# Kernel tuning notes

Measured on AMD Instinct MI355X. Metric: run time of the kernel, lower is better.

Reference implementation:

```python
import jax, jax.numpy as jnp
import numpy as np

B, L, H, K = 16, 65536, 64, 64


def setup_inputs() -> dict:
    key = jax.random.key(0)
    k1, k2 = jax.random.split(key, 2)
    x = jax.random.normal(k1, (B, L), dtype=jnp.float32)
    W = jax.random.normal(k2, (K, H), dtype=jnp.float32) * 0.02  # nn.Linear weight [K, H]
    b = jnp.zeros((K,), dtype=jnp.float32)
    return {"x": x, "W": W, "b": b}


def reference(x, W, b):
    # x: [B, L]; W: [K, H]; b: [K]
    Hh = W.shape[1]
    Bb, Ll = x.shape
    xpad = jnp.pad(x, ((0, 0), (Hh - 1, 0)))  # left-pad like F.pad(x, (H-1, 0))
    # Hankel windows: windows[b, t, j] = xpad[b, t + j]  -> [B, L, H]
    idx = jnp.arange(Ll)[:, None] + jnp.arange(Hh)[None, :]
    windows = xpad[:, idx]
    mu = windows.mean(axis=2, keepdims=True)
    sd = windows.std(axis=2, keepdims=True, ddof=1)  # torch std is unbiased (ddof=1)
    wn = (windows - mu) / (sd + 1e-6)
    d2 = jax.nn.relu(jnp.einsum('blh,kh->blk', wn, W) + b)
    warmup = Hh - 1
    return (d2[:, warmup:, :], warmup)
```

## Files before the change

kernel.cpp:

```cpp
#include <hip/hip_runtime.h>
#include <hip/hip_bf16.h>
#include <stdint.h>

#define LCOUNT 65536
#define LOUT   65473
#define KF     64
#define HH     64
#define TL     1024
#define ROW4   1104

typedef __attribute__((ext_vector_type(8))) short  short8;
typedef __attribute__((ext_vector_type(4))) short  short4v;
typedef __attribute__((ext_vector_type(4))) float  float4v;
typedef __attribute__((ext_vector_type(2))) float  float2v;

__device__ __forceinline__ unsigned short f2bf(float f) {
    union { float f; uint32_t u; } c; c.f = f;
    uint32_t u = c.u;
    u += 0x7FFFu + ((u >> 16) & 1u);
    return (unsigned short)(u >> 16);
}

__global__ __launch_bounds__(256, 4)
void hankel_kernel(const float* __restrict__ x,
                   const float* __restrict__ W,
                   const float* __restrict__ bias,
                   float* __restrict__ out)
{
    __shared__ __align__(16) float          xs_f[TL + 64];
    __shared__ __align__(16) unsigned short rep4[4 * ROW4];
    __shared__ __align__(16) float          muinv_s[2 * TL];
    __shared__ float wsum_s[KF];
    __shared__ float bias_s[KF];

    const int tid  = threadIdx.x;
    const int lane = tid & 63;
    const int wv   = tid >> 6;
    const int m    = lane & 15;
    const int quad = lane >> 4;

    const int tile     = blockIdx.x;
    const int bb       = blockIdx.y;
    const int block_lo = tile * TL;

    {
        const float4v* xrow4 = (const float4v*)(x + (size_t)bb * LCOUNT);
        const int base4 = block_lo >> 2;
        const int nf4   = (TL + 64) / 4;
        for (int i4 = tid; i4 < nf4; i4 += 256) {
            int g4 = base4 + i4;
            if (g4 > LCOUNT / 4 - 1) g4 = LCOUNT / 4 - 1;
            float4v v = xrow4[g4];
            *(float4v*)(xs_f + 4 * i4) = v;
            uint32_t plo = (uint32_t)f2bf(v[0]) | ((uint32_t)f2bf(v[1]) << 16);
            uint32_t phi = (uint32_t)f2bf(v[2]) | ((uint32_t)f2bf(v[3]) << 16);
            *(uint2*)(rep4 + 4 * i4) = make_uint2(plo, phi);
        }
    }

    if (tid < KF) {
        const float4v* wr = (const float4v*)(W + tid * HH);
        float s = 0.f;
        #pragma unroll
        for (int i = 0; i < HH / 4; ++i) {
            float4v w = wr[i];
            s += w[0] + w[1] + w[2] + w[3];
        }
        wsum_s[tid] = s;
        bias_s[tid] = bias[tid];
    }

    short8 afrag[4][2];
    #pragma unroll
    for (int t = 0; t < 4; ++t) {
        const int k = t * 16 + m;
        #pragma unroll
        for (int ki = 0; ki < 2; ++ki) {
            const float4v* wp = (const float4v*)(W + k * HH + quad * 8 + ki * 32);
            float4v w0 = wp[0];
            float4v w1 = wp[1];
            short8 f;
            f[0] = (short)f2bf(w0[0]); f[1] = (short)f2bf(w0[1]);
            f[2] = (short)f2bf(w0[2]); f[3] = (short)f2bf(w0[3]);
            f[4] = (short)f2bf(w1[0]); f[5] = (short)f2bf(w1[1]);
            f[6] = (short)f2bf(w1[2]); f[7] = (short)f2bf(w1[3]);
            afrag[t][ki] = f;
        }
    }

    __syncthreads();

    {
        const int p0 = 4 * tid;
        const float4v* xv = (const float4v*)(xs_f + p0);
        float s1 = 0.f, s2 = 0.f;
        float4v v0 = xv[0];
        float4v v16 = xv[16];
        #pragma unroll
        for (int i = 0; i < 16; ++i) {
            float4v v = xv[i];
            s1 += v[0] + v[1] + v[2] + v[3];
            s2 += v[0] * v[0] + v[1] * v[1] + v[2] * v[2] + v[3] * v[3];
        }
        float mu4[4], inv4[4];
        #pragma unroll
        for (int i = 0; i < 4; ++i) {
            if (i > 0) {
                float xo = v0[i - 1], xn = v16[i - 1];
                s1 += xn - xo;
                s2 += xn * xn - xo * xo;
            }
            float mu  = s1 * (1.f / 64.f);
            float var = (s2 - 64.f * mu * mu) * (1.f / 63.f);
            var = var < 0.f ? 0.f : var;
            mu4[i]  = mu;
            inv4[i] = 1.f / (sqrtf(var) + 1e-6f);
        }
        float4v lo4, hi4;
        lo4[0] = mu4[0]; lo4[1] = inv4[0]; lo4[2] = mu4[1]; lo4[3] = inv4[1];
        hi4[0] = mu4[2]; hi4[1] = inv4[2]; hi4[2] = mu4[3]; hi4[3] = inv4[3];
        *(float4v*)(muinv_s + 8 * tid)     = lo4;
        *(float4v*)(muinv_s + 8 * tid + 4) = hi4;
    }

    for (int tt = tid; tt < 544; tt += 256) {
        const int s = tt & 3;
        const int c = tt >> 2;
        if (s) {
            const int i0 = 8 * c + s;
            short8 w;
            #pragma unroll
            for (int j = 0; j < 8; ++j) w[j] = (short)rep4[i0 + j];
            *(short8*)(rep4 + s * ROW4 + 8 * c) = w;
        }
    }
    __syncthreads();

    const unsigned short* myrow = rep4 + (m & 3) * ROW4 + (m & 12) + quad * 8;
    float* const outb = out + (size_t)bb * LOUT * KF + quad * 4;

    for (int gg = wv; gg < TL / 16; gg += 8) {
        float4v pay[2][4];
        #pragma unroll
        for (int u = 0; u < 2; ++u) {
            const int g  = gg + 4 * u;
            const int p0 = g * 16;

            short4v a0 = *(const short4v*)(myrow + p0);
            short4v a1 = *(const short4v*)(myrow + p0 + 4);
            short4v a2 = *(const short4v*)(myrow + p0 + 32);
            short4v a3 = *(const short4v*)(myrow + p0 + 36);
            short8 b0 = __builtin_shufflevector(a0, a1, 0, 1, 2, 3, 4, 5, 6, 7);
            short8 b1 = __builtin_shufflevector(a2, a3, 0, 1, 2, 3, 4, 5, 6, 7);

            float2v mi = *(const float2v*)(muinv_s + 2 * (p0 + m));
            const float invv = mi[1];
            const float nmi  = -mi[0] * invv;

            float4v acc[4];
            #pragma unroll
            for (int t = 0; t < 4; ++t) acc[t] = (float4v){0.f, 0.f, 0.f, 0.f};
            #pragma unroll
            for (int t = 0; t < 4; ++t) {
                acc[t] = __builtin_amdgcn_mfma_f32_16x16x32_bf16(afrag[t][0], b0, acc[t], 0, 0, 0);
                acc[t] = __builtin_amdgcn_mfma_f32_16x16x32_bf16(afrag[t][1], b1, acc[t], 0, 0, 0);
            }

            #pragma unroll
            for (int t = 0; t < 4; ++t) {
                float4v ws = *(const float4v*)(wsum_s + t * 16 + quad * 4);
                float4v bs = *(const float4v*)(bias_s + t * 16 + quad * 4);
                #pragma unroll
                for (int r = 0; r < 4; ++r) {
                    float vv = fmaf(acc[t][r], invv, fmaf(nmi, ws[r], bs[r]));
                    pay[u][t][r] = vv > 0.f ? vv : 0.f;
                }
            }

            const int pos = block_lo + p0 + m;
            if (pos < LOUT) {
                float* op = outb + (size_t)pos * KF;
                #pragma unroll
                for (int t = 0; t < 4; ++t)
                    __builtin_nontemporal_store(pay[u][t], (float4v*)(op + t * 16));
            }
        }
    }

    if (tile == 0 && bb == 0 && tid == 0) {
        out[(size_t)16 * LOUT * KF] = 63.0f;
    }
}

extern "C" void kernel_launch(void* const* d_in, const int* in_sizes, int n_in,
                              void* d_out, int out_size, void* d_ws, size_t ws_size,
                              hipStream_t stream) {
    const float* x = (const float*)d_in[0];
    const float* W = (const float*)d_in[1];
    const float* b = (const float*)d_in[2];
    float* out = (float*)d_out;

    dim3 grid((LOUT + TL - 1) / TL, 16);
    hankel_kernel<<<grid, 256, 0, stream>>>(x, W, b, out);
}
```

Before: 311.7 us.

## Halve tile size, raise occupancy, and use plain stores instead of nontemporal

Shrinks the per-block tile from 1024 to 512 positions and raises the launch-bounds occupancy hint from 4 to 8 blocks per CU. The shared-memory setup loops become single guarded passes. The main loop drops the two-group software unroll and processes one 16-position group per iteration, storing each result right after compute with regular stores instead of nontemporal stores. The aim is more concurrent blocks to hide latency on this store-bound kernel, at the cost of more halo reloads, more per-block setup, and losing the nontemporal cache hint.

New measurement: 368.9 us. +18.3%, slower.

```diff
diff --git a/kernel.cpp b/kernel.cpp
--- a/kernel.cpp
+++ b/kernel.cpp
@@ -6,8 +6,8 @@
 #define LOUT   65473
 #define KF     64
 #define HH     64
-#define TL     1024
-#define ROW4   1104
+#define TL     512
+#define ROW4   592
 
 typedef __attribute__((ext_vector_type(8))) short  short8;
 typedef __attribute__((ext_vector_type(4))) short  short4v;
@@ -21,7 +21,7 @@
     return (unsigned short)(u >> 16);
 }
 
-__global__ __launch_bounds__(256, 4)
+__global__ __launch_bounds__(256, 8)
 void hankel_kernel(const float* __restrict__ x,
                    const float* __restrict__ W,
                    const float* __restrict__ bias,
@@ -47,14 +47,14 @@
         const float4v* xrow4 = (const float4v*)(x + (size_t)bb * LCOUNT);
         const int base4 = block_lo >> 2;
         const int nf4   = (TL + 64) / 4;
-        for (int i4 = tid; i4 < nf4; i4 += 256) {
-            int g4 = base4 + i4;
+        if (tid < nf4) {
+            int g4 = base4 + tid;
             if (g4 > LCOUNT / 4 - 1) g4 = LCOUNT / 4 - 1;
             float4v v = xrow4[g4];
-            *(float4v*)(xs_f + 4 * i4) = v;
+            *(float4v*)(xs_f + 4 * tid) = v;
             uint32_t plo = (uint32_t)f2bf(v[0]) | ((uint32_t)f2bf(v[1]) << 16);
             uint32_t phi = (uint32_t)f2bf(v[2]) | ((uint32_t)f2bf(v[3]) << 16);
-            *(uint2*)(rep4 + 4 * i4) = make_uint2(plo, phi);
+            *(uint2*)(rep4 + 4 * tid) = make_uint2(plo, phi);
         }
     }
 
@@ -90,7 +90,7 @@
 
     __syncthreads();
 
-    {
+    if (tid < TL / 4) {
         const int p0 = 4 * tid;
         const float4v* xv = (const float4v*)(xs_f + p0);
         float s1 = 0.f, s2 = 0.f;
@@ -123,66 +123,59 @@
         *(float4v*)(muinv_s + 8 * tid + 4) = hi4;
     }
 
-    for (int tt = tid; tt < 544; tt += 256) {
-        const int s = tt & 3;
-        const int c = tt >> 2;
-        if (s) {
-            const int i0 = 8 * c + s;
-            short8 w;
-            #pragma unroll
-            for (int j = 0; j < 8; ++j) w[j] = (short)rep4[i0 + j];
-            *(short8*)(rep4 + s * ROW4 + 8 * c) = w;
-        }
+    if (tid < 216) {
+        const int c = tid / 3;
+        const int s = 1 + tid % 3;
+        const int i0 = 8 * c + s;
+        short8 w;
+        #pragma unroll
+        for (int j = 0; j < 8; ++j) w[j] = (short)rep4[i0 + j];
+        *(short8*)(rep4 + s * ROW4 + 8 * c) = w;
     }
     __syncthreads();
 
     const unsigned short* myrow = rep4 + (m & 3) * ROW4 + (m & 12) + quad * 8;
     float* const outb = out + (size_t)bb * LOUT * KF + quad * 4;
 
-    for (int gg = wv; gg < TL / 16; gg += 8) {
-        float4v pay[2][4];
+    const bool full = (block_lo + TL) <= LOUT;
+
+    for (int g = wv; g < TL / 16; g += 4) {
+        const int p0 = g * 16;
+
+        short4v a0 = *(const short4v*)(myrow + p0);
+        short4v a1 = *(const short4v*)(myrow + p0 + 4);
+        short4v a2 = *(const short4v*)(myrow + p0 + 32);
+        short4v a3 = *(const short4v*)(myrow + p0 + 36);
+        short8 b0 = __builtin_shufflevector(a0, a1, 0, 1, 2, 3, 4, 5, 6, 7);
+        short8 b1 = __builtin_shufflevector(a2, a3, 0, 1, 2, 3, 4, 5, 6, 7);
+
+        float2v mi = *(const float2v*)(muinv_s + 2 * (p0 + m));
+        const float invv = mi[1];
+        const float nmi  = -mi[0] * invv;
+
+        float4v acc[4];
         #pragma unroll
-        for (int u = 0; u < 2; ++u) {
-            const int g  = gg + 4 * u;
-            const int p0 = g * 16;
+        for (int t = 0; t < 4; ++t) acc[t] = (float4v){0.f, 0.f, 0.f, 0.f};
+        #pragma unroll
+        for (int t = 0; t < 4; ++t) {
+            acc[t] = __builtin_amdgcn_mfma_f32_16x16x32_bf16(afrag[t][0], b0, acc[t], 0, 0, 0);
+            acc[t] = __builtin_amdgcn_mfma_f32_16x16x32_bf16(afrag[t][1], b1, acc[t], 0, 0, 0);
+        }
 
-            short4v a0 = *(const short4v*)(myrow + p0);
-            short4v a1 = *(const short4v*)(myrow + p0 + 4);
-            short4v a2 = *(const short4v*)(myrow + p0 + 32);
-            short4v a3 = *(const short4v*)(myrow + p0 + 36);
-            short8 b0 = __builtin_shufflevector(a0, a1, 0, 1, 2, 3, 4, 5, 6, 7);
-            short8 b1 = __builtin_shufflevector(a2, a3, 0, 1, 2, 3, 4, 5, 6, 7);
-
-            float2v mi = *(const float2v*)(muinv_s + 2 * (p0 + m));
-            const float invv = mi[1];
-            const float nmi  = -mi[0] * invv;
-
-            float4v acc[4];
-            #pragma unroll
-            for (int t = 0; t < 4; ++t) acc[t] = (float4v){0.f, 0.f, 0.f, 0.f};
-            #pragma unroll
-            for (int t = 0; t < 4; ++t) {
-                acc[t] = __builtin_amdgcn_mfma_f32_16x16x32_bf16(afrag[t][0], b0, acc[t], 0, 0, 0);
-                acc[t] = __builtin_amdgcn_mfma_f32_16x16x32_bf16(afrag[t][1], b1, acc[t], 0, 0, 0);
-            }
-
+        const int pos = block_lo + p0 + m;
+        float* op = outb + (size_t)pos * KF;
+        if (full | (pos < LOUT)) {
             #pragma unroll
             for (int t = 0; t < 4; ++t) {
                 float4v ws = *(const float4v*)(wsum_s + t * 16 + quad * 4);
                 float4v bs = *(const float4v*)(bias_s + t * 16 + quad * 4);
+                float4v v;
                 #pragma unroll
                 for (int r = 0; r < 4; ++r) {
                     float vv = fmaf(acc[t][r], invv, fmaf(nmi, ws[r], bs[r]));
-                    pay[u][t][r] = vv > 0.f ? vv : 0.f;
+                    v[r] = vv > 0.f ? vv : 0.f;
                 }
-            }
-
-            const int pos = block_lo + p0 + m;
-            if (pos < LOUT) {
-                float* op = outb + (size_t)pos * KF;
-                #pragma unroll
-                for (int t = 0; t < 4; ++t)
-                    __builtin_nontemporal_store(pay[u][t], (float4v*)(op + t * 16));
+                *(float4v*)(op + t * 16) = v;
             }
         }
     }
```
